# Performance work log

Measured on AMD Instinct MI355X. Metric: run time of the kernel, lower is better.

The kernel has to match this reference:

```python
import jax, jax.numpy as jnp
import numpy as np

DIM = 1280
BATCH = 65536


def setup_inputs() -> dict:
    key = jax.random.key(0)
    # diffusion-style timesteps in [0, 1000)
    time = jax.random.uniform(key, (BATCH,), dtype=jnp.float32) * 1000.0
    return {"time": time}


def reference(time) -> jnp.ndarray:
    # angle_rads[b, i] = time[b] / 10000 ** (2 * (i // 2) / dim)
    i = jnp.arange(DIM)
    power = (2.0 * (i // 2).astype(jnp.float32)) / DIM          # [dim]
    angle_rate = jnp.power(jnp.float32(10000.0), -power)        # [dim]
    ang = time[:, None] * angle_rate[None, :]                   # [B, dim]
    # even indices -> sin, odd indices -> cos
    out = jnp.where((i % 2 == 0)[None, :], jnp.sin(ang), jnp.cos(ang))
    return out  # [B, dim]
```

## Files before the change

### kernel.cpp

```cpp
#include <hip/hip_runtime.h>
#include <math.h>

#define DIM 1280
#define BATCH_THREADS 320

__global__ __launch_bounds__(BATCH_THREADS)
void time_emb_kernel(const float* __restrict__ time, float* __restrict__ out, int batch) {
    const int t = threadIdx.x;
    const float L_over_640 = 13.287712379549449f / 640.0f;
    const float rate0 = exp2f(-(float)(2 * t)     * L_over_640);
    const float rate1 = exp2f(-(float)(2 * t + 1) * L_over_640);

    for (int b = blockIdx.x; b < batch; b += gridDim.x) {
        const float tv = time[b];
        float s0, c0, s1, c1;
        __sincosf(tv * rate0, &s0, &c0);
        __sincosf(tv * rate1, &s1, &c1);
        float4 v = make_float4(s0, c0, s1, c1);
        *reinterpret_cast<float4*>(out + (size_t)b * DIM + (t << 2)) = v;
    }
}

extern "C" void kernel_launch(void* const* d_in, const int* in_sizes, int n_in,
                              void* d_out, int out_size, void* d_ws, size_t ws_size,
                              hipStream_t stream) {
    const float* time = (const float*)d_in[0];
    float* out = (float*)d_out;
    const int batch = in_sizes[0];

    const int grid = 2048;
    time_emb_kernel<<<grid, BATCH_THREADS, 0, stream>>>(time, out, batch);
}
```

Baseline: 66.40 us.

## Flatten thread mapping to global float4 index with grid-stride unrolled loop

Replaces the one-block-per-row mapping (320 threads per row) with a flat global thread index over all float4 output elements, using 256-thread blocks and a fixed grid of 2560. Each thread keeps a constant column, so its two angle rates are computed once, and it steps rows by 2048 per iteration with an unroll of 4. The aim is more stores in flight and simpler addressing for a write-bandwidth-bound kernel. It relies on the grid stride being an exact multiple of the row width, which ties it to the hardcoded constants.

```diff
diff --git a/kernel.cpp b/kernel.cpp
--- a/kernel.cpp
+++ b/kernel.cpp
@@ -2,22 +2,30 @@
 #include <math.h>
 
 #define DIM 1280
-#define BATCH_THREADS 320
+#define COL4 320
+#define NT 256
+#define GRID 2560
 
-__global__ __launch_bounds__(BATCH_THREADS)
-void time_emb_kernel(const float* __restrict__ time, float* __restrict__ out, int batch) {
-    const int t = threadIdx.x;
+typedef float f32x4 __attribute__((ext_vector_type(4)));
+
+__global__ __launch_bounds__(NT)
+void time_emb_kernel(const float* __restrict__ time, f32x4* __restrict__ out4, int total4) {
+    const int tid = blockIdx.x * NT + threadIdx.x;
+    const int col4 = tid % COL4;
+    int b = tid / COL4;
+
     const float L_over_640 = 13.287712379549449f / 640.0f;
-    const float rate0 = exp2f(-(float)(2 * t)     * L_over_640);
-    const float rate1 = exp2f(-(float)(2 * t + 1) * L_over_640);
+    const float rate0 = exp2f(-(float)(2 * col4)     * L_over_640);
+    const float rate1 = exp2f(-(float)(2 * col4 + 1) * L_over_640);
 
-    for (int b = blockIdx.x; b < batch; b += gridDim.x) {
+    #pragma unroll 4
+    for (int idx = tid; idx < total4; idx += GRID * NT, b += 2048) {
         const float tv = time[b];
         float s0, c0, s1, c1;
         __sincosf(tv * rate0, &s0, &c0);
         __sincosf(tv * rate1, &s1, &c1);
-        float4 v = make_float4(s0, c0, s1, c1);
-        *reinterpret_cast<float4*>(out + (size_t)b * DIM + (t << 2)) = v;
+        f32x4 v; v.x = s0; v.y = c0; v.z = s1; v.w = c1;
+        out4[idx] = v;
     }
 }
 
@@ -25,9 +33,9 @@
                               void* d_out, int out_size, void* d_ws, size_t ws_size,
                               hipStream_t stream) {
     const float* time = (const float*)d_in[0];
-    float* out = (float*)d_out;
+    f32x4* out4 = (f32x4*)d_out;
     const int batch = in_sizes[0];
+    const int total4 = batch * COL4;
 
-    const int grid = 2048;
-    time_emb_kernel<<<grid, BATCH_THREADS, 0, stream>>>(time, out, batch);
+    time_emb_kernel<<<GRID, NT, 0, stream>>>(time, out4, total4);
 }
```

Measured after the change: 65.00 us. -2.1%, faster.
